# Optimization experiments

Measured on AMD Instinct MI355X. Metric: run time of the kernel, lower is better.

The kernel has to match this reference:

```python
import jax, jax.numpy as jnp
import numpy as np

EPS = 1e-5

def _ln(x, s, b):
    m = jnp.mean(x, axis=-1, keepdims=True)
    v = jnp.mean((x - m) ** 2, axis=-1, keepdims=True)
    return (x - m) * jax.lax.rsqrt(v + EPS) * s + b

def _lin(x, w, b):
    # torch nn.Linear: y = x @ w.T + b, w shape (out, in)
    return jnp.einsum('...i,oi->...o', x, w) + b

def _gelu(x):
    return jax.nn.gelu(x, approximate=False)  # torch nn.GELU default (erf)

def setup_inputs() -> dict:
    key = jax.random.key(0)
    L, B, N, P, D, F, H = 4, 16, 8, 64, 128, 128, 8
    ks = jax.random.split(key, 16)
    nrm = lambda k, s: jax.random.normal(k, s, jnp.float32) * 0.02
    return {
        'sequence': jax.random.normal(ks[0], (B, N, P, D), jnp.float32),
        'H_pre': jax.random.normal(ks[1], (L, B, N, P, D), jnp.float32),
        'pro1_w': nrm(ks[2], (L, F, D)), 'pro1_b': jnp.zeros((L, F), jnp.float32),
        'pro2_w': nrm(ks[3], (L, F, D)), 'pro2_b': jnp.zeros((L, F), jnp.float32),
        'ln_cur_s': jnp.ones((L, F), jnp.float32), 'ln_cur_b': jnp.zeros((L, F), jnp.float32),
        'ln_pre_s': jnp.ones((L, F), jnp.float32), 'ln_pre_b': jnp.zeros((L, F), jnp.float32),
        'cur_qkv_w': nrm(ks[4], (L, 3 * H * F, F)), 'cur_qkv_b': jnp.zeros((L, 3 * H * F), jnp.float32),
        'pre_qkv_w': nrm(ks[5], (L, 3 * H * F, F)), 'pre_qkv_b': jnp.zeros((L, 3 * H * F), jnp.float32),
        'alpha': jax.random.uniform(ks[6], (L, 3, H * F), jnp.float32),
        'proj_w': nrm(ks[7], (L, F, H * F)), 'proj_b': jnp.zeros((L, F), jnp.float32),
        'bn1_s': jnp.ones((L, F), jnp.float32), 'bn1_b': jnp.zeros((L, F), jnp.float32),
        'bn2_s': jnp.ones((L, F), jnp.float32), 'bn2_b': jnp.zeros((L, F), jnp.float32),
        'ln_o_s': jnp.ones((L, F), jnp.float32), 'ln_o_b': jnp.zeros((L, F), jnp.float32),
        'ffn_w': nrm(ks[8], (L, F, F)), 'ffn_b': jnp.zeros((L, F), jnp.float32),
    }

def reference(sequence, H_pre, pro1_w, pro1_b, pro2_w, pro2_b, ln_cur_s, ln_cur_b,
              ln_pre_s, ln_pre_b, cur_qkv_w, cur_qkv_b, pre_qkv_w, pre_qkv_b, alpha,
              proj_w, proj_b, bn1_s, bn1_b, bn2_s, bn2_b, ln_o_s, ln_o_b, ffn_w, ffn_b):
    L = H_pre.shape[0]
    F = ffn_w.shape[-1]
    H = cur_qkv_w.shape[1] // (3 * F)
    scale = F ** -0.5  # Recur_self_attn: dim ** -0.5 with dim = ffn_dim

    def qkv(x, w, b):
        y = _lin(x, w, b)                      # (B, N, P, 3*H*F)
        Bq, Nq, Pq, _ = y.shape
        y = y.reshape(Bq, Nq, Pq, 3, H, F)     # matches 'b n (qkv h d)' split order
        y = jnp.transpose(y, (3, 0, 1, 4, 2, 5))  # (3, B, N, H, P, F)
        return y[0], y[1], y[2]

    cur = sequence  # (B, N, P, D); timesteps are independent in this module -> batched over N
    for l in range(L):
        if l == 0:  # only first cell sees last-dim == dim and projects cur
            cur = _ln(_lin(cur, pro1_w[l], pro1_b[l]), ln_cur_s[l], ln_cur_b[l])
        pre = _ln(_lin(H_pre[l], pro2_w[l], pro2_b[l]), ln_pre_s[l], ln_pre_b[l])

        Qc, Kc, Vc = qkv(cur, cur_qkv_w[l], cur_qkv_b[l])
        Qp, Kp, Vp = qkv(pre, pre_qkv_w[l], pre_qkv_b[l])
        a = jax.nn.sigmoid(alpha[l]).reshape(3, H, F)[:, None, None, :, None, :]  # (3,1,1,H,1,F)
        Q = a[0] * Qc + (1.0 - a[0]) * Qp
        K = a[1] * Kc + (1.0 - a[1]) * Kp
        V = a[2] * Vc + (1.0 - a[2]) * Vp

        attn = jax.nn.softmax(jnp.einsum('bnhpf,bnhqf->bnhpq', Q, K) * scale, axis=-1)
        A = jnp.einsum('bnhpq,bnhqf->bnhpf', attn, V)
        A = _ln(A, bn1_s[l], bn1_b[l])
        Bx, Nx, Hx, Px, Fx = A.shape
        A = jnp.transpose(A, (0, 1, 3, 2, 4)).reshape(Bx, Nx, Px, Hx * Fx)  # 'b h n d -> b n (h d)'
        A = _ln(_lin(A, proj_w[l], proj_b[l]), bn2_s[l], bn2_b[l])
        A = A + _gelu(cur)

        O_hat = _ln(cur + A, ln_o_s[l], ln_o_b[l])
        cur = _lin(O_hat, ffn_w[l], ffn_b[l]) + _gelu(O_hat)
    return cur
```

## Files before the change

kernel.cpp:

```cpp
#include <hip/hip_runtime.h>
#include <math.h>

#define EPS 1e-5f


typedef __bf16 bf16x8 __attribute__((ext_vector_type(8)));
typedef __bf16 bf16x4 __attribute__((ext_vector_type(4)));
typedef float f32x4 __attribute__((ext_vector_type(4)));

#define MFMA16 __builtin_amdgcn_mfma_f32_16x16x32_bf16

__device__ __forceinline__ float gelu_f(float x) {
    return 0.5f * x * (1.0f + erff(x * 0.7071067811865476f));
}

__device__ __forceinline__ void gll16(const void* g, void* l) {
    __builtin_amdgcn_global_load_lds(
        (const __attribute__((address_space(1))) void*)g,
        (__attribute__((address_space(3))) void*)l, 16, 0, 0);
}

__device__ __forceinline__ void cvt_store8(void* dst, const float* __restrict__ src) {
    float4 a = ((const float4*)src)[0];
    float4 b = ((const float4*)src)[1];
    bf16x8 v;
    v[0] = (__bf16)a.x; v[1] = (__bf16)a.y; v[2] = (__bf16)a.z; v[3] = (__bf16)a.w;
    v[4] = (__bf16)b.x; v[5] = (__bf16)b.y; v[6] = (__bf16)b.z; v[7] = (__bf16)b.w;
    *(bf16x8*)dst = v;
}

__device__ __forceinline__ int swz(int row, int k0)   { return row * 128 + (k0 ^ ((row & 7) << 3)); }
__device__ __forceinline__ int swz64(int row, int k0) { return row * 64  + (k0 ^ ((row & 7) << 3)); }

__global__ __launch_bounds__(256) void build_wq(
    const float* __restrict__ Wc, const float* __restrict__ bc,
    const float* __restrict__ Wp, const float* __restrict__ bp,
    const float* __restrict__ alpha,
    __bf16* __restrict__ Wq, float* __restrict__ bq)
{
    int idx = blockIdx.x * 256 + threadIdx.x;
    int l = idx / 98304, rem = idx - l * 98304;
    int row = rem >> 5, g = rem & 31, k0 = g << 3;
    int type = row >> 10, hf = row & 1023, h = hf >> 7, f = hf & 127;
    int rowp = h * 384 + type * 128 + f;
    float a = 1.0f / (1.0f + expf(-alpha[l * 3072 + row]));
    __bf16* dst = Wq + ((size_t)l * 3072 + rowp) * 256 + k0;
    if (k0 < 128) {
        const float* s = Wc + ((size_t)l * 3072 + row) * 128 + k0;
#pragma unroll
        for (int j = 0; j < 8; ++j) dst[j] = (__bf16)(a * s[j]);
    } else {
        const float* s = Wp + ((size_t)l * 3072 + row) * 128 + (k0 - 128);
#pragma unroll
        for (int j = 0; j < 8; ++j) dst[j] = (__bf16)((1.0f - a) * s[j]);
    }
    if (g == 0)
        bq[l * 3072 + rowp] = a * bc[l * 3072 + row] + (1.0f - a) * bp[l * 3072 + row];
}

__global__ __launch_bounds__(256) void cvt_all(
    const float* __restrict__ s0, __bf16* __restrict__ d0, int n0,
    const float* __restrict__ s1, __bf16* __restrict__ d1, int n1,
    const float* __restrict__ s2, __bf16* __restrict__ d2, int n2,
    const float* __restrict__ s3, __bf16* __restrict__ d3, int n3)
{
    int off = (blockIdx.x * 256 + threadIdx.x) * 4;
    const float* s; __bf16* d;
    if (off < n0) { s = s0; d = d0; }
    else {
        off -= n0;
        if (off < n1) { s = s1; d = d1; }
        else {
            off -= n1;
            if (off < n2) { s = s2; d = d2; }
            else {
                off -= n2;
                if (off >= n3) return;
                s = s3; d = d3;
            }
        }
    }
    float4 v = *(const float4*)(s + off);
    d[off] = (__bf16)v.x; d[off + 1] = (__bf16)v.y;
    d[off + 2] = (__bf16)v.z; d[off + 3] = (__bf16)v.w;
}

__global__ __launch_bounds__(256) void lin_pre_all(
    const float* __restrict__ Hpre, const __bf16* __restrict__ Wb,
    const float* __restrict__ bias, const float* __restrict__ lns_g,
    const float* __restrict__ lnb_g, __bf16* __restrict__ preb)
{
    __shared__ __align__(16) char lds[40960];
    unsigned short* xs = (unsigned short*)lds;
    unsigned short* ws = (unsigned short*)(lds + 8192);
    float* outs = (float*)lds;
    int l = blockIdx.x >> 8;
    int R = (blockIdx.x & 255) * 32;
    const float* x = Hpre + (size_t)l * 8192 * 128;
    const __bf16* Wbf = Wb + (size_t)l * 16384;
    const float* bias_l = bias + l * 128;
    const float* lns = lns_g + l * 128;
    const float* lnb = lnb_g + l * 128;
    __bf16* Xout = preb + (size_t)l * 8192 * 128;
    int t = threadIdx.x;
#pragma unroll
    for (int i = 0; i < 2; ++i) {
        int c = t + i * 256; int row = c >> 4, k0 = (c & 15) << 3;
        cvt_store8(&xs[swz(row, k0)], x + (size_t)(R + row) * 128 + k0);
    }
#pragma unroll
    for (int i = 0; i < 8; ++i) {
        int c = t + i * 256; int row = c >> 4, k0 = (c & 15) << 3;
        gll16(Wbf + (size_t)row * 128 + (k0 ^ ((row & 7) << 3)), &ws[c * 8]);
    }
    __syncthreads();
    int lane = t & 63, w = t >> 6;
    int wr = (w >> 1) * 16, wcol = (w & 1) * 64;
    int fr = lane & 15, fk = (lane >> 4) << 3;
    f32x4 acc[4] = {};
#pragma unroll
    for (int kk = 0; kk < 4; ++kk) {
        int k0 = kk * 32 + fk;
        bf16x8 a = *(const bf16x8*)&xs[swz(wr + fr, k0)];
#pragma unroll
        for (int n = 0; n < 4; ++n) {
            bf16x8 b = *(const bf16x8*)&ws[swz(wcol + n * 16 + fr, k0)];
            acc[n] = MFMA16(a, b, acc[n], 0, 0, 0);
        }
    }
    __syncthreads();
#pragma unroll
    for (int n = 0; n < 4; ++n) {
        int col = wcol + n * 16 + fr;
        float bv = bias_l[col];
        int rl = wr + ((lane >> 4) << 2);
#pragma unroll
        for (int r = 0; r < 4; ++r) outs[(rl + r) * 132 + col] = acc[n][r] + bv;
    }
    __syncthreads();
    int row = t >> 3, oc = t & 7;
    float vals[16]; float s = 0.0f;
#pragma unroll
    for (int i = 0; i < 16; ++i) { vals[i] = outs[row * 132 + oc + 8 * i]; s += vals[i]; }
    s += __shfl_xor(s, 1, 8); s += __shfl_xor(s, 2, 8); s += __shfl_xor(s, 4, 8);
    float mean = s * (1.0f / 128.0f);
    float sq = 0.0f;
#pragma unroll
    for (int i = 0; i < 16; ++i) { float d = vals[i] - mean; sq += d * d; }
    sq += __shfl_xor(sq, 1, 8); sq += __shfl_xor(sq, 2, 8); sq += __shfl_xor(sq, 4, 8);
    float rs = rsqrtf(sq * (1.0f / 128.0f) + EPS);
#pragma unroll
    for (int i = 0; i < 16; ++i) {
        int c = oc + 8 * i;
        Xout[(size_t)(R + row) * 128 + c] = (__bf16)((vals[i] - mean) * rs * lns[c] + lnb[c]);
    }
}

__global__ __launch_bounds__(256) void lin_ln_mfma(
    const float* __restrict__ x, const __bf16* __restrict__ Wbf,
    const float* __restrict__ bias, const float* __restrict__ lns,
    const float* __restrict__ lnb,
    float* __restrict__ yf, __bf16* __restrict__ Xout)
{
    __shared__ __align__(16) char lds[40960];
    unsigned short* xs = (unsigned short*)lds;
    unsigned short* ws = (unsigned short*)(lds + 8192);
    float* outs = (float*)lds;
    int t = threadIdx.x;
    int R = blockIdx.x * 32;
#pragma unroll
    for (int i = 0; i < 2; ++i) {
        int c = t + i * 256; int row = c >> 4, k0 = (c & 15) << 3;
        cvt_store8(&xs[swz(row, k0)], x + (size_t)(R + row) * 128 + k0);
    }
#pragma unroll
    for (int i = 0; i < 8; ++i) {
        int c = t + i * 256; int row = c >> 4, k0 = (c & 15) << 3;
        gll16(Wbf + (size_t)row * 128 + (k0 ^ ((row & 7) << 3)), &ws[c * 8]);
    }
    __syncthreads();
    int lane = t & 63, w = t >> 6;
    int wr = (w >> 1) * 16, wcol = (w & 1) * 64;
    int fr = lane & 15, fk = (lane >> 4) << 3;
    f32x4 acc[4] = {};
#pragma unroll
    for (int kk = 0; kk < 4; ++kk) {
        int k0 = kk * 32 + fk;
        bf16x8 a = *(const bf16x8*)&xs[swz(wr + fr, k0)];
#pragma unroll
        for (int n = 0; n < 4; ++n) {
            bf16x8 b = *(const bf16x8*)&ws[swz(wcol + n * 16 + fr, k0)];
            acc[n] = MFMA16(a, b, acc[n], 0, 0, 0);
        }
    }
    __syncthreads();
#pragma unroll
    for (int n = 0; n < 4; ++n) {
        int col = wcol + n * 16 + fr;
        float bv = bias[col];
        int rl = wr + ((lane >> 4) << 2);
#pragma unroll
        for (int r = 0; r < 4; ++r) outs[(rl + r) * 132 + col] = acc[n][r] + bv;
    }
    __syncthreads();
    int row = t >> 3, oc = t & 7;
    float vals[16]; float s = 0.0f;
#pragma unroll
    for (int i = 0; i < 16; ++i) { vals[i] = outs[row * 132 + oc + 8 * i]; s += vals[i]; }
    s += __shfl_xor(s, 1, 8); s += __shfl_xor(s, 2, 8); s += __shfl_xor(s, 4, 8);
    float mean = s * (1.0f / 128.0f);
    float sq = 0.0f;
#pragma unroll
    for (int i = 0; i < 16; ++i) { float d = vals[i] - mean; sq += d * d; }
    sq += __shfl_xor(sq, 1, 8); sq += __shfl_xor(sq, 2, 8); sq += __shfl_xor(sq, 4, 8);
    float rs = rsqrtf(sq * (1.0f / 128.0f) + EPS);
#pragma unroll
    for (int i = 0; i < 16; ++i) {
        int c = oc + 8 * i;
        float yv = (vals[i] - mean) * rs * lns[c] + lnb[c];
        yf[(size_t)(R + row) * 128 + c] = yv;
        Xout[(size_t)(R + row) * 128 + c] = (__bf16)yv;
    }
}

__global__ __launch_bounds__(256, 2) void qkv_attn(
    const __bf16* __restrict__ Xc, const __bf16* __restrict__ Pre,
    const __bf16* __restrict__ Wq, const float* __restrict__ bq,
    const float* __restrict__ bn1s, const float* __restrict__ bn1b,
    __bf16* __restrict__ At)
{
    __shared__ __align__(16) char lds[81920];
    unsigned short* Xs = (unsigned short*)lds;
    __bf16* Qs  = (__bf16*)lds;
    __bf16* Ks  = (__bf16*)(lds + 16384);
    __bf16* Vts = (__bf16*)(lds + 32768);
    __bf16* Ps  = (__bf16*)lds;

    int bn = blockIdx.x >> 3, h = blockIdx.x & 7;
    int t = threadIdx.x, lane = t & 63, w = t >> 6;
    int fr = lane & 15, fk = (lane >> 4) << 3;
    int rr = (lane >> 4) << 2;
    int w16 = w * 16;
    const __bf16* Wqh = Wq + (size_t)h * 384 * 256;
    const float* bqh = bq + h * 384;
    unsigned short* slab = (unsigned short*)(lds + 32768 + w * 12288);

#pragma unroll
    for (int i = 0; i < 8; ++i) {
        int c = t + i * 256;
        int row = c >> 5, k0 = (c & 31) << 3;
        int ks = k0 ^ ((row & 7) << 3);
        const __bf16* src = (ks < 128)
            ? Xc + (size_t)(bn * 64 + row) * 128 + ks
            : Pre + (size_t)(bn * 64 + row) * 128 + (ks - 128);
        gll16(src, &Xs[c * 8]);
    }
#pragma unroll
    for (int i = 0; i < 12; ++i) {
        int c = lane + i * 64;
        int rl = c >> 3, k0 = (c & 7) << 3;
        gll16(Wqh + (size_t)(w * 96 + rl) * 256 + 0 * 64 + (k0 ^ ((rl & 7) << 3)),
              &slab[c * 8]);
    }
    __syncthreads();

    f32x4 acc[4][6] = {};
    for (int kc = 0; kc < 4; ++kc) {
        if (kc) {
            asm volatile("s_waitcnt lgkmcnt(0)" ::: "memory");
#pragma unroll
            for (int i = 0; i < 12; ++i) {
                int c = lane + i * 64;
                int rl = c >> 3, k0 = (c & 7) << 3;
                gll16(Wqh + (size_t)(w * 96 + rl) * 256 + kc * 64 + (k0 ^ ((rl & 7) << 3)),
                      &slab[c * 8]);
            }
        }
        asm volatile("s_waitcnt vmcnt(0)" ::: "memory");
        __builtin_amdgcn_sched_barrier(0);
#pragma unroll
        for (int kk = 0; kk < 2; ++kk) {
            int kl = kk * 32 + fk;
            int kg = kc * 64 + kl;
            bf16x8 a[4], b[6];
#pragma unroll
            for (int m = 0; m < 4; ++m) {
                int row = m * 16 + fr;
                a[m] = *(const bf16x8*)&Xs[row * 256 + (kg ^ ((fr & 7) << 3))];
            }
#pragma unroll
            for (int n = 0; n < 6; ++n) {
                int rl = n * 16 + fr;
                b[n] = *(const bf16x8*)&slab[rl * 64 + (kl ^ ((fr & 7) << 3))];
            }
#pragma unroll
            for (int m = 0; m < 4; ++m)
#pragma unroll
                for (int n = 0; n < 6; ++n)
                    acc[m][n] = MFMA16(a[m], b[n], acc[m][n], 0, 0, 0);
        }
    }
    __syncthreads();

#pragma unroll
    for (int n = 0; n < 6; ++n) {
        int colb = w * 96 + n * 16;
        int type = colb >> 7;
        float bv = bqh[colb + fr];
        int f = (colb & 127) + fr;
#pragma unroll
        for (int m = 0; m < 4; ++m) {
            if (type == 2) {
                int rbase = m * 16 + rr;
                bf16x4 pk;
#pragma unroll
                for (int r = 0; r < 4; ++r) pk[r] = (__bf16)(acc[m][n][r] + bv);
                *(bf16x4*)&Vts[f * 64 + (rbase ^ ((f & 7) << 3))] = pk;
            } else {
#pragma unroll
                for (int r = 0; r < 4; ++r) {
                    int row = m * 16 + rr + r;
                    float val = acc[m][n][r] + bv;
                    if (type == 0)
                        Qs[row * 128 + (f ^ ((row & 7) << 3))] = (__bf16)val;
                    else
                        Ks[row * 128 + (f ^ ((row & 7) << 3))] = (__bf16)val;
                }
            }
        }
    }
    __syncthreads();

    f32x4 sacc[4] = {};
#pragma unroll
    for (int kk = 0; kk < 4; ++kk) {
        int k0 = kk * 32 + fk;
        int arow = w16 + fr;
        bf16x8 aq = *(const bf16x8*)&Qs[arow * 128 + (k0 ^ ((arow & 7) << 3))];
#pragma unroll
        for (int n = 0; n < 4; ++n) {
            bf16x8 bk = *(const bf16x8*)&Ks[swz(n * 16 + fr, k0)];
            sacc[n] = MFMA16(aq, bk, sacc[n], 0, 0, 0);
        }
    }
    __syncthreads();

    const float scale = 0.08838834764831845f;
#pragma unroll
    for (int r = 0; r < 4; ++r) {
        float sv[4];
#pragma unroll
        for (int n = 0; n < 4; ++n) sv[n] = sacc[n][r] * scale;
        float mx = fmaxf(fmaxf(sv[0], sv[1]), fmaxf(sv[2], sv[3]));
        mx = fmaxf(mx, __shfl_xor(mx, 1, 16));
        mx = fmaxf(mx, __shfl_xor(mx, 2, 16));
        mx = fmaxf(mx, __shfl_xor(mx, 4, 16));
        mx = fmaxf(mx, __shfl_xor(mx, 8, 16));
        float sum = 0.0f;
#pragma unroll
        for (int n = 0; n < 4; ++n) { sv[n] = expf(sv[n] - mx); sum += sv[n]; }
        sum += __shfl_xor(sum, 1, 16);
        sum += __shfl_xor(sum, 2, 16);
        sum += __shfl_xor(sum, 4, 16);
        sum += __shfl_xor(sum, 8, 16);
        float inv = 1.0f / sum;
        int p = w16 + rr + r;
#pragma unroll
        for (int n = 0; n < 4; ++n) {
            int q = n * 16 + fr;
            Ps[p * 64 + (q ^ ((p & 7) << 3))] = (__bf16)(sv[n] * inv);
        }
    }

    f32x4 oacc[8] = {};
#pragma unroll
    for (int kk = 0; kk < 2; ++kk) {
        int k0 = kk * 32 + fk;
        int arow = w16 + fr;
        bf16x8 ap = *(const bf16x8*)&Ps[arow * 64 + (k0 ^ ((arow & 7) << 3))];
#pragma unroll
        for (int n = 0; n < 8; ++n) {
            bf16x8 bv = *(const bf16x8*)&Vts[swz64(n * 16 + fr, k0)];
            oacc[n] = MFMA16(ap, bv, oacc[n], 0, 0, 0);
        }
    }

#pragma unroll
    for (int r = 0; r < 4; ++r) {
        int p = w16 + rr + r;
        float s1 = 0.0f;
#pragma unroll
        for (int n = 0; n < 8; ++n) s1 += oacc[n][r];
        s1 += __shfl_xor(s1, 1, 16);
        s1 += __shfl_xor(s1, 2, 16);
        s1 += __shfl_xor(s1, 4, 16);
        s1 += __shfl_xor(s1, 8, 16);
        float mean = s1 * (1.0f / 128.0f);
        float s2 = 0.0f;
#pragma unroll
        for (int n = 0; n < 8; ++n) { float d = oacc[n][r] - mean; s2 += d * d; }
        s2 += __shfl_xor(s2, 1, 16);
        s2 += __shfl_xor(s2, 2, 16);
        s2 += __shfl_xor(s2, 4, 16);
        s2 += __shfl_xor(s2, 8, 16);
        float rs = rsqrtf(s2 * (1.0f / 128.0f) + EPS);
        __bf16* orow = At + (size_t)(bn * 64 + p) * 1024 + h * 128;
#pragma unroll
        for (int n = 0; n < 8; ++n) {
            int f = n * 16 + fr;
            orow[f] = (__bf16)((oacc[n][r] - mean) * rs * bn1s[f] + bn1b[f]);
        }
    }
}

__global__ __launch_bounds__(256) void proj_ffn_mfma(
    const __bf16* __restrict__ At_g, const __bf16* __restrict__ Wp,
    const float* __restrict__ pb,
    const float* __restrict__ bn2s, const float* __restrict__ bn2b,
    const float* __restrict__ lnos, const float* __restrict__ lnob,
    const __bf16* __restrict__ Wf, const float* __restrict__ fb,
    const float* __restrict__ cur, float* __restrict__ out,
    __bf16* __restrict__ Xcur)
{
    __shared__ __align__(16) char lds[36864];
    unsigned short* ats = (unsigned short*)lds;
    unsigned short* wts = (unsigned short*)(lds + 4096);
    float* outs = (float*)lds;
    int t = threadIdx.x;
    int R = blockIdx.x * 16;
    int lane = t & 63, w = t >> 6;
    int wcol = w * 32;
    int fr = lane & 15, fk = (lane >> 4) << 3;
    int rr = (lane >> 4) << 2;

    f32x4 acc[2] = {};
    for (int kc = 0; kc < 8; ++kc) {
        {
            int row = t >> 4, k0 = (t & 15) << 3;
            gll16(At_g + (size_t)(R + row) * 1024 + kc * 128 + (k0 ^ ((row & 7) << 3)),
                  &ats[t * 8]);
        }
#pragma unroll
        for (int i = 0; i < 8; ++i) {
            int c = t + i * 256; int row = c >> 4, k0 = (c & 15) << 3;
            gll16(Wp + (size_t)row * 1024 + kc * 128 + (k0 ^ ((row & 7) << 3)),
                  &wts[c * 8]);
        }
        __syncthreads();
#pragma unroll
        for (int kk = 0; kk < 4; ++kk) {
            int k0 = kk * 32 + fk;
            bf16x8 a = *(const bf16x8*)&ats[swz(fr, k0)];
#pragma unroll
            for (int n = 0; n < 2; ++n) {
                bf16x8 b = *(const bf16x8*)&wts[swz(wcol + n * 16 + fr, k0)];
                acc[n] = MFMA16(a, b, acc[n], 0, 0, 0);
            }
        }
        __syncthreads();
    }

#pragma unroll
    for (int n = 0; n < 2; ++n) {
        int col = wcol + n * 16 + fr;
        float bv = pb[col];
#pragma unroll
        for (int r = 0; r < 4; ++r) outs[(rr + r) * 132 + col] = acc[n][r] + bv;
    }
    __syncthreads();

    int row = t >> 4, oc = t & 15;
    float vals[8]; float s = 0.0f;
#pragma unroll
    for (int i = 0; i < 8; ++i) { vals[i] = outs[row * 132 + oc + 16 * i]; s += vals[i]; }
    s += __shfl_xor(s, 1, 16); s += __shfl_xor(s, 2, 16);
    s += __shfl_xor(s, 4, 16); s += __shfl_xor(s, 8, 16);
    float mean = s * (1.0f / 128.0f);
    float sq = 0.0f;
#pragma unroll
    for (int i = 0; i < 8; ++i) { float d = vals[i] - mean; sq += d * d; }
    sq += __shfl_xor(sq, 1, 16); sq += __shfl_xor(sq, 2, 16);
    sq += __shfl_xor(sq, 4, 16); sq += __shfl_xor(sq, 8, 16);
    float rs = rsqrtf(sq * (1.0f / 128.0f) + EPS);

    float oh[8]; float s2 = 0.0f;
#pragma unroll
    for (int i = 0; i < 8; ++i) {
        int c = oc + 16 * i;
        float ynorm = (vals[i] - mean) * rs * bn2s[c] + bn2b[c];
        float cv = cur[(size_t)(R + row) * 128 + c];
        oh[i] = cv + (ynorm + gelu_f(cv));
        s2 += oh[i];
    }
    s2 += __shfl_xor(s2, 1, 16); s2 += __shfl_xor(s2, 2, 16);
    s2 += __shfl_xor(s2, 4, 16); s2 += __shfl_xor(s2, 8, 16);
    float mean2 = s2 * (1.0f / 128.0f);
    float sq2 = 0.0f;
#pragma unroll
    for (int i = 0; i < 8; ++i) { float d = oh[i] - mean2; sq2 += d * d; }
    sq2 += __shfl_xor(sq2, 1, 16); sq2 += __shfl_xor(sq2, 2, 16);
    sq2 += __shfl_xor(sq2, 4, 16); sq2 += __shfl_xor(sq2, 8, 16);
    float rs2 = rsqrtf(sq2 * (1.0f / 128.0f) + EPS);
#pragma unroll
    for (int i = 0; i < 8; ++i) {
        int c = oc + 16 * i;
        oh[i] = (oh[i] - mean2) * rs2 * lnos[c] + lnob[c];
    }
    __syncthreads();

#pragma unroll
    for (int i = 0; i < 8; ++i) {
        int c = oc + 16 * i;
        ((__bf16*)ats)[row * 128 + (c ^ ((row & 7) << 3))] = (__bf16)oh[i];
    }
#pragma unroll
    for (int i = 0; i < 8; ++i) {
        int c = t + i * 256; int rw = c >> 4, k0 = (c & 15) << 3;
        gll16(Wf + (size_t)rw * 128 + (k0 ^ ((rw & 7) << 3)), &wts[c * 8]);
    }
    __syncthreads();

    f32x4 acc2[2] = {};
#pragma unroll
    for (int kk = 0; kk < 4; ++kk) {
        int k0 = kk * 32 + fk;
        bf16x8 a = *(const bf16x8*)&ats[swz(fr, k0)];
#pragma unroll
        for (int n = 0; n < 2; ++n) {
            bf16x8 b = *(const bf16x8*)&wts[swz(wcol + n * 16 + fr, k0)];
            acc2[n] = MFMA16(a, b, acc2[n], 0, 0, 0);
        }
    }
#pragma unroll
    for (int n = 0; n < 2; ++n) {
        int col = wcol + n * 16 + fr;
        float bv = fb[col];
#pragma unroll
        for (int r = 0; r < 4; ++r) {
            int ro = rr + r;
            float ov = (float)((__bf16*)ats)[ro * 128 + (col ^ ((ro & 7) << 3))];
            float val = acc2[n][r] + bv + gelu_f(ov);
            size_t gidx = (size_t)(R + ro) * 128 + col;
            out[gidx] = val;
            if (Xcur) Xcur[gidx] = (__bf16)val;
        }
    }
}

extern "C" void kernel_launch(void* const* d_in, const int* in_sizes, int n_in,
                              void* d_out, int out_size, void* d_ws, size_t ws_size,
                              hipStream_t stream)
{
    const float* seq       = (const float*)d_in[0];
    const float* Hpre      = (const float*)d_in[1];
    const float* pro1_w    = (const float*)d_in[2];
    const float* pro1_b    = (const float*)d_in[3];
    const float* pro2_w    = (const float*)d_in[4];
    const float* pro2_b    = (const float*)d_in[5];
    const float* ln_cur_s  = (const float*)d_in[6];
    const float* ln_cur_b  = (const float*)d_in[7];
    const float* ln_pre_s  = (const float*)d_in[8];
    const float* ln_pre_b  = (const float*)d_in[9];
    const float* cur_qkv_w = (const float*)d_in[10];
    const float* cur_qkv_b = (const float*)d_in[11];
    const float* pre_qkv_w = (const float*)d_in[12];
    const float* pre_qkv_b = (const float*)d_in[13];
    const float* alpha     = (const float*)d_in[14];
    const float* proj_w    = (const float*)d_in[15];
    const float* proj_b    = (const float*)d_in[16];
    const float* bn1_s     = (const float*)d_in[17];
    const float* bn1_b     = (const float*)d_in[18];
    const float* bn2_s     = (const float*)d_in[19];
    const float* bn2_b     = (const float*)d_in[20];
    const float* ln_o_s    = (const float*)d_in[21];
    const float* ln_o_b    = (const float*)d_in[22];
    const float* ffn_w     = (const float*)d_in[23];
    const float* ffn_b     = (const float*)d_in[24];

    char* ws = (char*)d_ws;
    __bf16* Wq      = (__bf16*)ws;                 ws += (size_t)4 * 3072 * 256 * 2;
    float*  bq      = (float*)ws;                  ws += (size_t)4 * 3072 * 4;
    __bf16* Wp_bf   = (__bf16*)ws;                 ws += (size_t)4 * 128 * 1024 * 2;
    __bf16* Wf_bf   = (__bf16*)ws;                 ws += (size_t)4 * 128 * 128 * 2;
    __bf16* pro1_bf = (__bf16*)ws;                 ws += (size_t)128 * 128 * 2;
    __bf16* pro2_bf = (__bf16*)ws;                 ws += (size_t)4 * 128 * 128 * 2;
    __bf16* Xc   = (__bf16*)ws;                    ws += (size_t)8192 * 128 * 2;
    __bf16* preb = (__bf16*)ws;                    ws += (size_t)4 * 8192 * 128 * 2;
    float*  cur  = (float*)ws;                     ws += (size_t)8192 * 128 * 4;
    __bf16* Atb  = (__bf16*)ws;                    ws += (size_t)8192 * 1024 * 2;

    build_wq<<<1536, 256, 0, stream>>>(cur_qkv_w, cur_qkv_b, pre_qkv_w, pre_qkv_b,
                                       alpha, Wq, bq);
    cvt_all<<<656, 256, 0, stream>>>(proj_w, Wp_bf, 4 * 128 * 1024,
                                     ffn_w, Wf_bf, 4 * 128 * 128,
                                     pro1_w, pro1_bf, 128 * 128,
                                     pro2_w, pro2_bf, 4 * 128 * 128);
    lin_pre_all<<<1024, 256, 0, stream>>>(Hpre, pro2_bf, pro2_b,
                                          ln_pre_s, ln_pre_b, preb);
    lin_ln_mfma<<<256, 256, 0, stream>>>(seq, pro1_bf, pro1_b,
                                         ln_cur_s, ln_cur_b, cur, Xc);

    for (int l = 0; l < 4; ++l) {
        qkv_attn<<<1024, 256, 0, stream>>>(
            Xc, preb + (size_t)l * 8192 * 128,
            Wq + (size_t)l * 3072 * 256, bq + l * 3072,
            bn1_s + l * 128, bn1_b + l * 128, Atb);
        float* outp = (l == 3) ? (float*)d_out : cur;
        proj_ffn_mfma<<<512, 256, 0, stream>>>(Atb,
                                               Wp_bf + (size_t)l * 128 * 1024,
                                               proj_b + l * 128,
                                               bn2_s + l * 128, bn2_b + l * 128,
                                               ln_o_s + l * 128, ln_o_b + l * 128,
                                               Wf_bf + (size_t)l * 16384,
                                               ffn_b + l * 128,
                                               cur, outp, (l == 3) ? nullptr : Xc);
    }
}
```

Measured before the change: 221.7 us.

## Merge prep kernels, fuse input projections, and process two heads per attention block

Weight conversion and QKV weight building are merged into one launch, and the pre/cur input projection plus layernorm kernels are merged into one launch with 64-row tiles. The qkv_attn kernel now handles two heads per block, loading the X slab once and reusing it across both heads, with Q/K/V buffers moved to a separate LDS region so they no longer alias X. This cuts launch count and redundant X loads. In exchange each block carries more serial work and there are half as many blocks, which may leave the GPU less evenly occupied.

```diff
diff --git a/kernel.cpp b/kernel.cpp
--- a/kernel.cpp
+++ b/kernel.cpp
@@ -32,193 +32,139 @@
 __device__ __forceinline__ int swz(int row, int k0)   { return row * 128 + (k0 ^ ((row & 7) << 3)); }
 __device__ __forceinline__ int swz64(int row, int k0) { return row * 64  + (k0 ^ ((row & 7) << 3)); }
 
-__global__ __launch_bounds__(256) void build_wq(
+__global__ __launch_bounds__(256) void prep_all(
     const float* __restrict__ Wc, const float* __restrict__ bc,
-    const float* __restrict__ Wp, const float* __restrict__ bp,
+    const float* __restrict__ Wpq, const float* __restrict__ bp,
     const float* __restrict__ alpha,
-    __bf16* __restrict__ Wq, float* __restrict__ bq)
-{
-    int idx = blockIdx.x * 256 + threadIdx.x;
-    int l = idx / 98304, rem = idx - l * 98304;
-    int row = rem >> 5, g = rem & 31, k0 = g << 3;
-    int type = row >> 10, hf = row & 1023, h = hf >> 7, f = hf & 127;
-    int rowp = h * 384 + type * 128 + f;
-    float a = 1.0f / (1.0f + expf(-alpha[l * 3072 + row]));
-    __bf16* dst = Wq + ((size_t)l * 3072 + rowp) * 256 + k0;
-    if (k0 < 128) {
-        const float* s = Wc + ((size_t)l * 3072 + row) * 128 + k0;
-#pragma unroll
-        for (int j = 0; j < 8; ++j) dst[j] = (__bf16)(a * s[j]);
-    } else {
-        const float* s = Wp + ((size_t)l * 3072 + row) * 128 + (k0 - 128);
-#pragma unroll
-        for (int j = 0; j < 8; ++j) dst[j] = (__bf16)((1.0f - a) * s[j]);
-    }
-    if (g == 0)
-        bq[l * 3072 + rowp] = a * bc[l * 3072 + row] + (1.0f - a) * bp[l * 3072 + row];
-}
-
-__global__ __launch_bounds__(256) void cvt_all(
+    __bf16* __restrict__ Wq, float* __restrict__ bq,
     const float* __restrict__ s0, __bf16* __restrict__ d0, int n0,
     const float* __restrict__ s1, __bf16* __restrict__ d1, int n1,
     const float* __restrict__ s2, __bf16* __restrict__ d2, int n2,
     const float* __restrict__ s3, __bf16* __restrict__ d3, int n3)
 {
-    int off = (blockIdx.x * 256 + threadIdx.x) * 4;
-    const float* s; __bf16* d;
-    if (off < n0) { s = s0; d = d0; }
-    else {
-        off -= n0;
-        if (off < n1) { s = s1; d = d1; }
+    int b = blockIdx.x;
+    if (b < 1536) {
+        int idx = b * 256 + threadIdx.x;
+        int l = idx / 98304, rem = idx - l * 98304;
+        int row = rem >> 5, g = rem & 31, k0 = g << 3;
+        int type = row >> 10, hf = row & 1023, h = hf >> 7, f = hf & 127;
+        int rowp = h * 384 + type * 128 + f;
+        float a = 1.0f / (1.0f + expf(-alpha[l * 3072 + row]));
+        __bf16* dst = Wq + ((size_t)l * 3072 + rowp) * 256 + k0;
+        if (k0 < 128) {
+            const float* s = Wc + ((size_t)l * 3072 + row) * 128 + k0;
+#pragma unroll
+            for (int j = 0; j < 8; ++j) dst[j] = (__bf16)(a * s[j]);
+        } else {
+            const float* s = Wpq + ((size_t)l * 3072 + row) * 128 + (k0 - 128);
+#pragma unroll
+            for (int j = 0; j < 8; ++j) dst[j] = (__bf16)((1.0f - a) * s[j]);
+        }
+        if (g == 0)
+            bq[l * 3072 + rowp] = a * bc[l * 3072 + row] + (1.0f - a) * bp[l * 3072 + row];
+    } else {
+        int off = ((b - 1536) * 256 + threadIdx.x) * 4;
+        const float* s; __bf16* d;
+        if (off < n0) { s = s0; d = d0; }
         else {
-            off -= n1;
-            if (off < n2) { s = s2; d = d2; }
+            off -= n0;
+            if (off < n1) { s = s1; d = d1; }
             else {
-                off -= n2;
-                if (off >= n3) return;
-                s = s3; d = d3;
-            }
-        }
-    }
-    float4 v = *(const float4*)(s + off);
-    d[off] = (__bf16)v.x; d[off + 1] = (__bf16)v.y;
-    d[off + 2] = (__bf16)v.z; d[off + 3] = (__bf16)v.w;
-}
-
-__global__ __launch_bounds__(256) void lin_pre_all(
-    const float* __restrict__ Hpre, const __bf16* __restrict__ Wb,
-    const float* __restrict__ bias, const float* __restrict__ lns_g,
-    const float* __restrict__ lnb_g, __bf16* __restrict__ preb)
+                off -= n1;
+                if (off < n2) { s = s2; d = d2; }
+                else {
+                    off -= n2;
+                    if (off >= n3) return;
+                    s = s3; d = d3;
+                }
+            }
+        }
+        float4 v = *(const float4*)(s + off);
+        d[off] = (__bf16)v.x; d[off + 1] = (__bf16)v.y;
+        d[off + 2] = (__bf16)v.z; d[off + 3] = (__bf16)v.w;
+    }
+}
+
+__global__ __launch_bounds__(256) void lin_all(
+    const float* __restrict__ Hpre, const __bf16* __restrict__ pro2b,
+    const float* __restrict__ pro2bias,
+    const float* __restrict__ lnps, const float* __restrict__ lnpb,
+    __bf16* __restrict__ preb,
+    const float* __restrict__ seq, const __bf16* __restrict__ pro1b,
+    const float* __restrict__ pro1bias,
+    const float* __restrict__ lncs, const float* __restrict__ lncb,
+    float* __restrict__ curf, __bf16* __restrict__ Xcb)
 {
-    __shared__ __align__(16) char lds[40960];
+    __shared__ __align__(16) char lds[49152];
     unsigned short* xs = (unsigned short*)lds;
-    unsigned short* ws = (unsigned short*)(lds + 8192);
+    unsigned short* ws = (unsigned short*)(lds + 16384);
     float* outs = (float*)lds;
-    int l = blockIdx.x >> 8;
-    int R = (blockIdx.x & 255) * 32;
-    const float* x = Hpre + (size_t)l * 8192 * 128;
-    const __bf16* Wbf = Wb + (size_t)l * 16384;
-    const float* bias_l = bias + l * 128;
-    const float* lns = lns_g + l * 128;
-    const float* lnb = lnb_g + l * 128;
-    __bf16* Xout = preb + (size_t)l * 8192 * 128;
-    int t = threadIdx.x;
-#pragma unroll
-    for (int i = 0; i < 2; ++i) {
+    int b = blockIdx.x, t = threadIdx.x;
+    const float* x; const __bf16* W; const float* bias;
+    const float* lns; const float* lnb;
+    float* yf = nullptr; __bf16* Xout; int R;
+    if (b < 512) {
+        int l = b >> 7; R = (b & 127) * 64;
+        x = Hpre + (size_t)l * 8192 * 128;
+        W = pro2b + (size_t)l * 16384;
+        bias = pro2bias + l * 128; lns = lnps + l * 128; lnb = lnpb + l * 128;
+        Xout = preb + (size_t)l * 8192 * 128;
+    } else {
+        R = (b - 512) * 64;
+        x = seq; W = pro1b; bias = pro1bias; lns = lncs; lnb = lncb;
+        yf = curf; Xout = Xcb;
+    }
+#pragma unroll
+    for (int i = 0; i < 4; ++i) {
         int c = t + i * 256; int row = c >> 4, k0 = (c & 15) << 3;
         cvt_store8(&xs[swz(row, k0)], x + (size_t)(R + row) * 128 + k0);
     }
 #pragma unroll
     for (int i = 0; i < 8; ++i) {
         int c = t + i * 256; int row = c >> 4, k0 = (c & 15) << 3;
-        gll16(Wbf + (size_t)row * 128 + (k0 ^ ((row & 7) << 3)), &ws[c * 8]);
+        gll16(W + (size_t)row * 128 + (k0 ^ ((row & 7) << 3)), &ws[c * 8]);
     }
     __syncthreads();
     int lane = t & 63, w = t >> 6;
-    int wr = (w >> 1) * 16, wcol = (w & 1) * 64;
+    int wr = w * 16;
     int fr = lane & 15, fk = (lane >> 4) << 3;
-    f32x4 acc[4] = {};
+    f32x4 acc[8] = {};
 #pragma unroll
     for (int kk = 0; kk < 4; ++kk) {
         int k0 = kk * 32 + fk;
         bf16x8 a = *(const bf16x8*)&xs[swz(wr + fr, k0)];
 #pragma unroll
-        for (int n = 0; n < 4; ++n) {
-            bf16x8 b = *(const bf16x8*)&ws[swz(wcol + n * 16 + fr, k0)];
-            acc[n] = MFMA16(a, b, acc[n], 0, 0, 0);
+        for (int n = 0; n < 8; ++n) {
+            bf16x8 bb = *(const bf16x8*)&ws[swz(n * 16 + fr, k0)];
+            acc[n] = MFMA16(a, bb, acc[n], 0, 0, 0);
         }
     }
     __syncthreads();
 #pragma unroll
-    for (int n = 0; n < 4; ++n) {
-        int col = wcol + n * 16 + fr;
-        float bv = bias_l[col];
+    for (int n = 0; n < 8; ++n) {
+        int col = n * 16 + fr;
+        float bv = bias[col];
         int rl = wr + ((lane >> 4) << 2);
 #pragma unroll
         for (int r = 0; r < 4; ++r) outs[(rl + r) * 132 + col] = acc[n][r] + bv;
     }
     __syncthreads();
-    int row = t >> 3, oc = t & 7;
-    float vals[16]; float s = 0.0f;
-#pragma unroll
-    for (int i = 0; i < 16; ++i) { vals[i] = outs[row * 132 + oc + 8 * i]; s += vals[i]; }
-    s += __shfl_xor(s, 1, 8); s += __shfl_xor(s, 2, 8); s += __shfl_xor(s, 4, 8);
+    int row = t >> 2, oc = t & 3;
+    float vals[32]; float s = 0.0f;
+#pragma unroll
+    for (int i = 0; i < 32; ++i) { vals[i] = outs[row * 132 + oc + 4 * i]; s += vals[i]; }
+    s += __shfl_xor(s, 1, 4); s += __shfl_xor(s, 2, 4);
     float mean = s * (1.0f / 128.0f);
     float sq = 0.0f;
 #pragma unroll
-    for (int i = 0; i < 16; ++i) { float d = vals[i] - mean; sq += d * d; }
-    sq += __shfl_xor(sq, 1, 8); sq += __shfl_xor(sq, 2, 8); sq += __shfl_xor(sq, 4, 8);
+    for (int i = 0; i < 32; ++i) { float d = vals[i] - mean; sq += d * d; }
+    sq += __shfl_xor(sq, 1, 4); sq += __shfl_xor(sq, 2, 4);
     float rs = rsqrtf(sq * (1.0f / 128.0f) + EPS);
 #pragma unroll
-    for (int i = 0; i < 16; ++i) {
-        int c = oc + 8 * i;
-        Xout[(size_t)(R + row) * 128 + c] = (__bf16)((vals[i] - mean) * rs * lns[c] + lnb[c]);
-    }
-}
-
-__global__ __launch_bounds__(256) void lin_ln_mfma(
-    const float* __restrict__ x, const __bf16* __restrict__ Wbf,
-    const float* __restrict__ bias, const float* __restrict__ lns,
-    const float* __restrict__ lnb,
-    float* __restrict__ yf, __bf16* __restrict__ Xout)
-{
-    __shared__ __align__(16) char lds[40960];
-    unsigned short* xs = (unsigned short*)lds;
-    unsigned short* ws = (unsigned short*)(lds + 8192);
-    float* outs = (float*)lds;
-    int t = threadIdx.x;
-    int R = blockIdx.x * 32;
-#pragma unroll
-    for (int i = 0; i < 2; ++i) {
-        int c = t + i * 256; int row = c >> 4, k0 = (c & 15) << 3;
-        cvt_store8(&xs[swz(row, k0)], x + (size_t)(R + row) * 128 + k0);
-    }
-#pragma unroll
-    for (int i = 0; i < 8; ++i) {
-        int c = t + i * 256; int row = c >> 4, k0 = (c & 15) << 3;
-        gll16(Wbf + (size_t)row * 128 + (k0 ^ ((row & 7) << 3)), &ws[c * 8]);
-    }
-    __syncthreads();
-    int lane = t & 63, w = t >> 6;
-    int wr = (w >> 1) * 16, wcol = (w & 1) * 64;
-    int fr = lane & 15, fk = (lane >> 4) << 3;
-    f32x4 acc[4] = {};
-#pragma unroll
-    for (int kk = 0; kk < 4; ++kk) {
-        int k0 = kk * 32 + fk;
-        bf16x8 a = *(const bf16x8*)&xs[swz(wr + fr, k0)];
-#pragma unroll
-        for (int n = 0; n < 4; ++n) {
-            bf16x8 b = *(const bf16x8*)&ws[swz(wcol + n * 16 + fr, k0)];
-            acc[n] = MFMA16(a, b, acc[n], 0, 0, 0);
-        }
-    }
-    __syncthreads();
-#pragma unroll
-    for (int n = 0; n < 4; ++n) {
-        int col = wcol + n * 16 + fr;
-        float bv = bias[col];
-        int rl = wr + ((lane >> 4) << 2);
-#pragma unroll
-        for (int r = 0; r < 4; ++r) outs[(rl + r) * 132 + col] = acc[n][r] + bv;
-    }
-    __syncthreads();
-    int row = t >> 3, oc = t & 7;
-    float vals[16]; float s = 0.0f;
-#pragma unroll
-    for (int i = 0; i < 16; ++i) { vals[i] = outs[row * 132 + oc + 8 * i]; s += vals[i]; }
-    s += __shfl_xor(s, 1, 8); s += __shfl_xor(s, 2, 8); s += __shfl_xor(s, 4, 8);
-    float mean = s * (1.0f / 128.0f);
-    float sq = 0.0f;
-#pragma unroll
-    for (int i = 0; i < 16; ++i) { float d = vals[i] - mean; sq += d * d; }
-    sq += __shfl_xor(sq, 1, 8); sq += __shfl_xor(sq, 2, 8); sq += __shfl_xor(sq, 4, 8);
-    float rs = rsqrtf(sq * (1.0f / 128.0f) + EPS);
-#pragma unroll
-    for (int i = 0; i < 16; ++i) {
-        int c = oc + 8 * i;
+    for (int i = 0; i < 32; ++i) {
+        int c = oc + 4 * i;
         float yv = (vals[i] - mean) * rs * lns[c] + lnb[c];
-        yf[(size_t)(R + row) * 128 + c] = yv;
+        if (yf) yf[(size_t)(R + row) * 128 + c] = yv;
         Xout[(size_t)(R + row) * 128 + c] = (__bf16)yv;
     }
 }
@@ -231,18 +177,16 @@
 {
     __shared__ __align__(16) char lds[81920];
     unsigned short* Xs = (unsigned short*)lds;
-    __bf16* Qs  = (__bf16*)lds;
-    __bf16* Ks  = (__bf16*)(lds + 16384);
-    __bf16* Vts = (__bf16*)(lds + 32768);
-    __bf16* Ps  = (__bf16*)lds;
-
-    int bn = blockIdx.x >> 3, h = blockIdx.x & 7;
+    __bf16* Qs  = (__bf16*)(lds + 32768);
+    __bf16* Ks  = (__bf16*)(lds + 49152);
+    __bf16* Vts = (__bf16*)(lds + 65536);
+    __bf16* Ps  = (__bf16*)(lds + 32768);
+
+    int bn = blockIdx.x >> 2, j = blockIdx.x & 3;
     int t = threadIdx.x, lane = t & 63, w = t >> 6;
     int fr = lane & 15, fk = (lane >> 4) << 3;
     int rr = (lane >> 4) << 2;
     int w16 = w * 16;
-    const __bf16* Wqh = Wq + (size_t)h * 384 * 256;
-    const float* bqh = bq + h * 384;
     unsigned short* slab = (unsigned short*)(lds + 32768 + w * 12288);
 
 #pragma unroll
@@ -255,160 +199,169 @@
             : Pre + (size_t)(bn * 64 + row) * 128 + (ks - 128);
         gll16(src, &Xs[c * 8]);
     }
-#pragma unroll
-    for (int i = 0; i < 12; ++i) {
-        int c = lane + i * 64;
-        int rl = c >> 3, k0 = (c & 7) << 3;
-        gll16(Wqh + (size_t)(w * 96 + rl) * 256 + 0 * 64 + (k0 ^ ((rl & 7) << 3)),
-              &slab[c * 8]);
-    }
-    __syncthreads();
-
-    f32x4 acc[4][6] = {};
-    for (int kc = 0; kc < 4; ++kc) {
-        if (kc) {
-            asm volatile("s_waitcnt lgkmcnt(0)" ::: "memory");
-#pragma unroll
-            for (int i = 0; i < 12; ++i) {
-                int c = lane + i * 64;
-                int rl = c >> 3, k0 = (c & 7) << 3;
-                gll16(Wqh + (size_t)(w * 96 + rl) * 256 + kc * 64 + (k0 ^ ((rl & 7) << 3)),
-                      &slab[c * 8]);
-            }
-        }
-        asm volatile("s_waitcnt vmcnt(0)" ::: "memory");
-        __builtin_amdgcn_sched_barrier(0);
+
+    for (int hh = 0; hh < 2; ++hh) {
+        int h = j * 2 + hh;
+        const __bf16* Wqh = Wq + (size_t)h * 384 * 256;
+        const float* bqh = bq + h * 384;
+
+        if (hh == 1) __syncthreads();
+#pragma unroll
+        for (int i = 0; i < 12; ++i) {
+            int c = lane + i * 64;
+            int rl = c >> 3, k0 = (c & 7) << 3;
+            gll16(Wqh + (size_t)(w * 96 + rl) * 256 + (k0 ^ ((rl & 7) << 3)),
+                  &slab[c * 8]);
+        }
+        if (hh == 0) __syncthreads();
+
+        f32x4 acc[4][6] = {};
+        for (int kc = 0; kc < 4; ++kc) {
+            if (kc) {
+                asm volatile("s_waitcnt lgkmcnt(0)" ::: "memory");
+#pragma unroll
+                for (int i = 0; i < 12; ++i) {
+                    int c = lane + i * 64;
+                    int rl = c >> 3, k0 = (c & 7) << 3;
+                    gll16(Wqh + (size_t)(w * 96 + rl) * 256 + kc * 64 +
+                              (k0 ^ ((rl & 7) << 3)),
+                          &slab[c * 8]);
+                }
+            }
+            asm volatile("s_waitcnt vmcnt(0)" ::: "memory");
+            __builtin_amdgcn_sched_barrier(0);
+#pragma unroll
+            for (int kk = 0; kk < 2; ++kk) {
+                int kl = kk * 32 + fk;
+                int kg = kc * 64 + kl;
+                bf16x8 a[4], b[6];
+#pragma unroll
+                for (int m = 0; m < 4; ++m) {
+                    int row = m * 16 + fr;
+                    a[m] = *(const bf16x8*)&Xs[row * 256 + (kg ^ ((fr & 7) << 3))];
+                }
+#pragma unroll
+                for (int n = 0; n < 6; ++n) {
+                    int rl = n * 16 + fr;
+                    b[n] = *(const bf16x8*)&slab[rl * 64 + (kl ^ ((fr & 7) << 3))];
+                }
+#pragma unroll
+                for (int m = 0; m < 4; ++m)
+#pragma unroll
+                    for (int n = 0; n < 6; ++n)
+                        acc[m][n] = MFMA16(a[m], b[n], acc[m][n], 0, 0, 0);
+            }
+        }
+        __syncthreads();
+
+#pragma unroll
+        for (int n = 0; n < 6; ++n) {
+            int colb = w * 96 + n * 16;
+            int type = colb >> 7;
+            float bv = bqh[colb + fr];
+            int f = (colb & 127) + fr;
+#pragma unroll
+            for (int m = 0; m < 4; ++m) {
+                if (type == 2) {
+                    int rbase = m * 16 + rr;
+                    bf16x4 pk;
+#pragma unroll
+                    for (int r = 0; r < 4; ++r) pk[r] = (__bf16)(acc[m][n][r] + bv);
+                    *(bf16x4*)&Vts[f * 64 + (rbase ^ ((f & 7) << 3))] = pk;
+                } else {
+#pragma unroll
+                    for (int r = 0; r < 4; ++r) {
+                        int row = m * 16 + rr + r;
+                        float val = acc[m][n][r] + bv;
+                        if (type == 0)
+                            Qs[row * 128 + (f ^ ((row & 7) << 3))] = (__bf16)val;
+                        else
+                            Ks[row * 128 + (f ^ ((row & 7) << 3))] = (__bf16)val;
+                    }
+                }
+            }
+        }
+        __syncthreads();
+
+        f32x4 sacc[4] = {};
+#pragma unroll
+        for (int kk = 0; kk < 4; ++kk) {
+            int k0 = kk * 32 + fk;
+            int arow = w16 + fr;
+            bf16x8 aq = *(const bf16x8*)&Qs[arow * 128 + (k0 ^ ((arow & 7) << 3))];
+#pragma unroll
+            for (int n = 0; n < 4; ++n) {
+                bf16x8 bk = *(const bf16x8*)&Ks[swz(n * 16 + fr, k0)];
+                sacc[n] = MFMA16(aq, bk, sacc[n], 0, 0, 0);
+            }
+        }
+        __syncthreads();
+
+        const float scale = 0.08838834764831845f;
+#pragma unroll
+        for (int r = 0; r < 4; ++r) {
+            float sv[4];
+#pragma unroll
+            for (int n = 0; n < 4; ++n) sv[n] = sacc[n][r] * scale;
+            float mx = fmaxf(fmaxf(sv[0], sv[1]), fmaxf(sv[2], sv[3]));
+            mx = fmaxf(mx, __shfl_xor(mx, 1, 16));
+            mx = fmaxf(mx, __shfl_xor(mx, 2, 16));
+            mx = fmaxf(mx, __shfl_xor(mx, 4, 16));
+            mx = fmaxf(mx, __shfl_xor(mx, 8, 16));
+            float sum = 0.0f;
+#pragma unroll
+            for (int n = 0; n < 4; ++n) { sv[n] = expf(sv[n] - mx); sum += sv[n]; }
+            sum += __shfl_xor(sum, 1, 16);
+            sum += __shfl_xor(sum, 2, 16);
+            sum += __shfl_xor(sum, 4, 16);
+            sum += __shfl_xor(sum, 8, 16);
+            float inv = 1.0f / sum;
+            int p = w16 + rr + r;
+#pragma unroll
+            for (int n = 0; n < 4; ++n) {
+                int q = n * 16 + fr;
+                Ps[p * 64 + (q ^ ((p & 7) << 3))] = (__bf16)(sv[n] * inv);
+            }
+        }
+
+        f32x4 oacc[8] = {};
 #pragma unroll
         for (int kk = 0; kk < 2; ++kk) {
-            int kl = kk * 32 + fk;
-            int kg = kc * 64 + kl;
-            bf16x8 a[4], b[6];
-#pragma unroll
-            for (int m = 0; m < 4; ++m) {
-                int row = m * 16 + fr;
-                a[m] = *(const bf16x8*)&Xs[row * 256 + (kg ^ ((fr & 7) << 3))];
-            }
-#pragma unroll
-            for (int n = 0; n < 6; ++n) {
-                int rl = n * 16 + fr;
-                b[n] = *(const bf16x8*)&slab[rl * 64 + (kl ^ ((fr & 7) << 3))];
-            }
-#pragma unroll
-            for (int m = 0; m < 4; ++m)
-#pragma unroll
-                for (int n = 0; n < 6; ++n)
-                    acc[m][n] = MFMA16(a[m], b[n], acc[m][n], 0, 0, 0);
-        }
-    }
-    __syncthreads();
-
-#pragma unroll
-    for (int n = 0; n < 6; ++n) {
-        int colb = w * 96 + n * 16;
-        int type = colb >> 7;
-        float bv = bqh[colb + fr];
-        int f = (colb & 127) + fr;
-#pragma unroll
-        for (int m = 0; m < 4; ++m) {
-            if (type == 2) {
-                int rbase = m * 16 + rr;
-                bf16x4 pk;
-#pragma unroll
-                for (int r = 0; r < 4; ++r) pk[r] = (__bf16)(acc[m][n][r] + bv);
-                *(bf16x4*)&Vts[f * 64 + (rbase ^ ((f & 7) << 3))] = pk;
-            } else {
-#pragma unroll
-                for (int r = 0; r < 4; ++r) {
-                    int row = m * 16 + rr + r;
-                    float val = acc[m][n][r] + bv;
-                    if (type == 0)
-                        Qs[row * 128 + (f ^ ((row & 7) << 3))] = (__bf16)val;
-                    else
-                        Ks[row * 128 + (f ^ ((row & 7) << 3))] = (__bf16)val;
-                }
-            }
-        }
-    }
-    __syncthreads();
-
-    f32x4 sacc[4] = {};
-#pragma unroll
-    for (int kk = 0; kk < 4; ++kk) {
-        int k0 = kk * 32 + fk;
-        int arow = w16 + fr;
-        bf16x8 aq = *(const bf16x8*)&Qs[arow * 128 + (k0 ^ ((arow & 7) << 3))];
-#pragma unroll
-        for (int n = 0; n < 4; ++n) {
-            bf16x8 bk = *(const bf16x8*)&Ks[swz(n * 16 + fr, k0)];
-            sacc[n] = MFMA16(aq, bk, sacc[n], 0, 0, 0);
-        }
-    }
-    __syncthreads();
-
-    const float scale = 0.08838834764831845f;
-#pragma unroll
-    for (int r = 0; r < 4; ++r) {
-        float sv[4];
-#pragma unroll
-        for (int n = 0; n < 4; ++n) sv[n] = sacc[n][r] * scale;
-        float mx = fmaxf(fmaxf(sv[0], sv[1]), fmaxf(sv[2], sv[3]));
-        mx = fmaxf(mx, __shfl_xor(mx, 1, 16));
-        mx = fmaxf(mx, __shfl_xor(mx, 2, 16));
-        mx = fmaxf(mx, __shfl_xor(mx, 4, 16));
-        mx = fmaxf(mx, __shfl_xor(mx, 8, 16));
-        float sum = 0.0f;
-#pragma unroll
-        for (int n = 0; n < 4; ++n) { sv[n] = expf(sv[n] - mx); sum += sv[n]; }
-        sum += __shfl_xor(sum, 1, 16);
-        sum += __shfl_xor(sum, 2, 16);
-        sum += __shfl_xor(sum, 4, 16);
-        sum += __shfl_xor(sum, 8, 16);
-        float inv = 1.0f / sum;
-        int p = w16 + rr + r;
-#pragma unroll
-        for (int n = 0; n < 4; ++n) {
-            int q = n * 16 + fr;
-            Ps[p * 64 + (q ^ ((p & 7) << 3))] = (__bf16)(sv[n] * inv);
-        }
-    }
-
-    f32x4 oacc[8] = {};
-#pragma unroll
-    for (int kk = 0; kk < 2; ++kk) {
-        int k0 = kk * 32 + fk;
-        int arow = w16 + fr;
-        bf16x8 ap = *(const bf16x8*)&Ps[arow * 64 + (k0 ^ ((arow & 7) << 3))];
-#pragma unroll
-        for (int n = 0; n < 8; ++n) {
-            bf16x8 bv = *(const bf16x8*)&Vts[swz64(n * 16 + fr, k0)];
-            oacc[n] = MFMA16(ap, bv, oacc[n], 0, 0, 0);
-        }
-    }
-
-#pragma unroll
-    for (int r = 0; r < 4; ++r) {
-        int p = w16 + rr + r;
-        float s1 = 0.0f;
-#pragma unroll
-        for (int n = 0; n < 8; ++n) s1 += oacc[n][r];
-        s1 += __shfl_xor(s1, 1, 16);
-        s1 += __shfl_xor(s1, 2, 16);
-        s1 += __shfl_xor(s1, 4, 16);
-        s1 += __shfl_xor(s1, 8, 16);
-        float mean = s1 * (1.0f / 128.0f);
-        float s2 = 0.0f;
-#pragma unroll
-        for (int n = 0; n < 8; ++n) { float d = oacc[n][r] - mean; s2 += d * d; }
-        s2 += __shfl_xor(s2, 1, 16);
-        s2 += __shfl_xor(s2, 2, 16);
-        s2 += __shfl_xor(s2, 4, 16);
-        s2 += __shfl_xor(s2, 8, 16);
-        float rs = rsqrtf(s2 * (1.0f / 128.0f) + EPS);
-        __bf16* orow = At + (size_t)(bn * 64 + p) * 1024 + h * 128;
-#pragma unroll
-        for (int n = 0; n < 8; ++n) {
-            int f = n * 16 + fr;
-            orow[f] = (__bf16)((oacc[n][r] - mean) * rs * bn1s[f] + bn1b[f]);
+            int k0 = kk * 32 + fk;
+            int arow = w16 + fr;
+            bf16x8 ap = *(const bf16x8*)&Ps[arow * 64 + (k0 ^ ((arow & 7) << 3))];
+#pragma unroll
+            for (int n = 0; n < 8; ++n) {
+                bf16x8 bv = *(const bf16x8*)&Vts[swz64(n * 16 + fr, k0)];
+                oacc[n] = MFMA16(ap, bv, oacc[n], 0, 0, 0);
+            }
+        }
+
+#pragma unroll
+        for (int r = 0; r < 4; ++r) {
+            int p = w16 + rr + r;
+            float s1 = 0.0f;
+#pragma unroll
+            for (int n = 0; n < 8; ++n) s1 += oacc[n][r];
+            s1 += __shfl_xor(s1, 1, 16);
+            s1 += __shfl_xor(s1, 2, 16);
+            s1 += __shfl_xor(s1, 4, 16);
+            s1 += __shfl_xor(s1, 8, 16);
+            float mean = s1 * (1.0f / 128.0f);
+            float s2 = 0.0f;
+#pragma unroll
+            for (int n = 0; n < 8; ++n) { float d = oacc[n][r] - mean; s2 += d * d; }
+            s2 += __shfl_xor(s2, 1, 16);
+            s2 += __shfl_xor(s2, 2, 16);
+            s2 += __shfl_xor(s2, 4, 16);
+            s2 += __shfl_xor(s2, 8, 16);
+            float rs = rsqrtf(s2 * (1.0f / 128.0f) + EPS);
+            __bf16* orow = At + (size_t)(bn * 64 + p) * 1024 + h * 128;
+#pragma unroll
+            for (int n = 0; n < 8; ++n) {
+                int f = n * 16 + fr;
+                orow[f] = (__bf16)((oacc[n][r] - mean) * rs * bn1s[f] + bn1b[f]);
+            }
         }
     }
 }
@@ -589,19 +542,18 @@
     float*  cur  = (float*)ws;                     ws += (size_t)8192 * 128 * 4;
     __bf16* Atb  = (__bf16*)ws;                    ws += (size_t)8192 * 1024 * 2;
 
-    build_wq<<<1536, 256, 0, stream>>>(cur_qkv_w, cur_qkv_b, pre_qkv_w, pre_qkv_b,
-                                       alpha, Wq, bq);
-    cvt_all<<<656, 256, 0, stream>>>(proj_w, Wp_bf, 4 * 128 * 1024,
-                                     ffn_w, Wf_bf, 4 * 128 * 128,
-                                     pro1_w, pro1_bf, 128 * 128,
-                                     pro2_w, pro2_bf, 4 * 128 * 128);
-    lin_pre_all<<<1024, 256, 0, stream>>>(Hpre, pro2_bf, pro2_b,
-                                          ln_pre_s, ln_pre_b, preb);
-    lin_ln_mfma<<<256, 256, 0, stream>>>(seq, pro1_bf, pro1_b,
-                                         ln_cur_s, ln_cur_b, cur, Xc);
+    prep_all<<<2192, 256, 0, stream>>>(
+        cur_qkv_w, cur_qkv_b, pre_qkv_w, pre_qkv_b, alpha, Wq, bq,
+        proj_w, Wp_bf, 4 * 128 * 1024,
+        ffn_w, Wf_bf, 4 * 128 * 128,
+        pro1_w, pro1_bf, 128 * 128,
+        pro2_w, pro2_bf, 4 * 128 * 128);
+    lin_all<<<640, 256, 0, stream>>>(Hpre, pro2_bf, pro2_b, ln_pre_s, ln_pre_b,
+                                     preb, seq, pro1_bf, pro1_b,
+                                     ln_cur_s, ln_cur_b, cur, Xc);
 
     for (int l = 0; l < 4; ++l) {
-        qkv_attn<<<1024, 256, 0, stream>>>(
+        qkv_attn<<<512, 256, 0, stream>>>(
             Xc, preb + (size_t)l * 8192 * 128,
             Wq + (size_t)l * 3072 * 256, bq + l * 3072,
             bn1_s + l * 128, bn1_b + l * 128, Atb);
```

New measurement: 454.1 us. +104.8%, slower.
